# Optimization experiments

Measured on AMD Instinct MI355X. Metric: run time of the kernel, lower is better.

Reference implementation:

```python
import jax, jax.numpy as jnp
import numpy as np

EPS = 1e-5

def _bn_relu(x, gamma, beta):
    # BatchNorm2d in training mode: biased batch stats over (B, H, W)
    mu = jnp.mean(x, axis=(0, 2, 3), keepdims=True)
    var = jnp.mean((x - mu) ** 2, axis=(0, 2, 3), keepdims=True)
    xh = (x - mu) * jax.lax.rsqrt(var + EPS)
    return jax.nn.relu(xh * gamma[None, :, None, None] + beta[None, :, None, None])

def setup_inputs() -> dict:
    key = jax.random.key(0)
    ks = jax.random.split(key, 16)
    B, N, D = 4, 256, 256            # in_channels = 2*D = 512
    feats = jax.random.normal(ks[0], (B, 1 + 2 * N, D), dtype=jnp.float32)
    def lin(k, o, c):
        return jax.random.normal(k, (o, c), dtype=jnp.float32) * (1.0 / np.sqrt(c))
    return {
        "feats": feats,
        "W1": lin(ks[1], 256, 512), "b1": jnp.zeros((256,), jnp.float32),
        "g1": jnp.ones((256,), jnp.float32), "be1": jnp.zeros((256,), jnp.float32),
        "W2": lin(ks[2], 128, 256), "b2": jnp.zeros((128,), jnp.float32),
        "g2": jnp.ones((128,), jnp.float32), "be2": jnp.zeros((128,), jnp.float32),
        "W3": lin(ks[3], 64, 128), "b3": jnp.zeros((64,), jnp.float32),
        "g3": jnp.ones((64,), jnp.float32), "be3": jnp.zeros((64,), jnp.float32),
        "W4": lin(ks[4], 1, 64), "b4": jnp.zeros((1,), jnp.float32),
    }

def reference(feats, W1, b1, g1, be1, W2, b2, g2, be2, W3, b3, g3, be3, W4, b4):
    B, T, Dfull = feats.shape
    f = feats[:, 1:]                                  # [B, 2N, D]
    N = f.shape[1] // 2
    D = f.shape[2]
    f = f.reshape(B, N, 2, D).mean(axis=2)            # [B, N, D]
    fc = jnp.transpose(f, (0, 2, 1))                  # [B, D, N]
    # conv1(cat(x, t)) fused: first D input channels see f_i, last D see f_j
    a = jnp.einsum('oc,bcn->bon', W1[:, :D], fc)      # [B, 256, N]
    bpart = jnp.einsum('oc,bcn->bon', W1[:, D:], fc)  # [B, 256, N]
    h = a[:, :, :, None] + bpart[:, :, None, :] + b1[None, :, None, None]  # [B,256,N,N]
    h = _bn_relu(h, g1, be1)
    h = jnp.einsum('oc,bcij->boij', W2, h) + b2[None, :, None, None]
    h = _bn_relu(h, g2, be2)
    h = jnp.einsum('oc,bcij->boij', W3, h) + b3[None, :, None, None]
    h = _bn_relu(h, g3, be3)
    h = jnp.einsum('oc,bcij->boij', W4, h) + b4[None, :, None, None]
    return h[:, 0]                                    # [B, N, N]
```

## Files before the change

kernel.cpp:

```cpp
#include <hip/hip_runtime.h>
#include <hip/hip_bf16.h>

#define EPS 1e-5f

typedef __attribute__((ext_vector_type(8))) short bf16x8;
typedef __attribute__((ext_vector_type(4))) float f32x4;

static constexpr size_t OFF_FT    = 0;
static constexpr size_t OFF_W1T   = 1048576;
static constexpr size_t OFF_W2B   = 1572864;
static constexpr size_t OFF_W3B   = 1638400;
static constexpr size_t OFF_S1    = 1654784;
static constexpr size_t OFF_T1    = 1655808;
static constexpr size_t OFF_S2    = 1658368;
static constexpr size_t OFF_T2    = 1658880;
static constexpr size_t OFF_S3    = 1659392;
static constexpr size_t OFF_T3    = 1659648;
static constexpr size_t OFF_ST2   = 1660928;
static constexpr size_t OFF_ST3   = 1669120;
static constexpr size_t OFF_ABT   = 1703936;
static constexpr size_t OFF_H2T   = 4194304;
static constexpr size_t OFF_P1    = OFF_H2T;
static constexpr size_t OFF_H3T   = 71303168;

static __device__ inline float bfu2f(unsigned int u16) {
    return __uint_as_float(u16 << 16);
}
static __device__ inline unsigned short f2bfu(float f) {
    unsigned int u = __float_as_uint(f);
    unsigned int r = u + 0x7fffu + ((u >> 16) & 1u);
    return (unsigned short)(r >> 16);
}
static __device__ inline unsigned int pkbf(float lo, float hi) {
    __hip_bfloat162 p = __float22bfloat162_rn(make_float2(lo, hi));
    return *reinterpret_cast<unsigned int*>(&p);
}

__global__ void k0_pairmean_T(const float* __restrict__ feats, float* __restrict__ fT) {
    __shared__ float s[64][65];
    int b = blockIdx.x >> 2;
    int n0 = (blockIdx.x & 3) * 64;
    int tid = threadIdx.x;
    const float* fb = feats + (size_t)b * 513 * 256;
    for (int c0 = 0; c0 < 256; c0 += 64) {
        for (int idx = tid; idx < 64 * 64; idx += 256) {
            int n = idx >> 6, c = idx & 63;
            const float* r = fb + (size_t)(1 + 2 * (n0 + n)) * 256 + c0 + c;
            s[n][c] = 0.5f * (r[0] + r[256]);
        }
        __syncthreads();
        for (int idx = tid; idx < 64 * 64; idx += 256) {
            int c = idx >> 6, n = idx & 63;
            fT[((size_t)b * 256 + c0 + c) * 256 + n0 + n] = s[n][c];
        }
        __syncthreads();
    }
}

__global__ void kt_prep(const float* __restrict__ W1, const float* __restrict__ W2,
                        const float* __restrict__ W3, float* __restrict__ W1T,
                        unsigned short* __restrict__ W2b, unsigned short* __restrict__ W3b) {
    int idx = blockIdx.x * 256 + threadIdx.x;
    if (idx < 131072) {
        int c = idx >> 9, o = idx & 511;
        W1T[idx] = (o < 256) ? W1[(size_t)o * 512 + c] : W1[(size_t)(o - 256) * 512 + 256 + c];
    } else if (idx < 163840) {
        int j = idx - 131072;
        W2b[j] = f2bfu(W2[j]);
    } else if (idx < 172032) {
        int j = idx - 163840;
        W3b[j] = f2bfu(W3[j]);
    }
}

__global__ __launch_bounds__(256) void k1_gemm(const float* __restrict__ W1T,
                                               const float* __restrict__ fT,
                                               float* __restrict__ abT,
                                               float2* __restrict__ part) {
    __shared__ float sW[64][68];
    __shared__ float sF[64][68];
    int tid = threadIdx.x;
    int b = blockIdx.x >> 2, n0 = (blockIdx.x & 3) * 64;
    int o0 = blockIdx.y * 64;
    int jq = tid & 15, og = tid >> 4;
    float acc[4][4] = {};
    for (int c0 = 0; c0 < 256; c0 += 64) {
        for (int idx = tid; idx < 64 * 64; idx += 256) {
            int c = idx >> 6, o = idx & 63;
            sW[c][o] = W1T[(size_t)(c0 + c) * 512 + o0 + o];
        }
        for (int idx = tid; idx < 64 * 64; idx += 256) {
            int c = idx >> 6, n = idx & 63;
            sF[c][n] = fT[((size_t)b * 256 + c0 + c) * 256 + n0 + n];
        }
        __syncthreads();
        #pragma unroll 8
        for (int c = 0; c < 64; ++c) {
            float4 rv = *(const float4*)&sF[c][jq * 4];
            float4 wv = *(const float4*)&sW[c][og * 4];
            float rr[4] = {rv.x, rv.y, rv.z, rv.w};
            float ww[4] = {wv.x, wv.y, wv.z, wv.w};
            #pragma unroll
            for (int m = 0; m < 4; ++m)
                #pragma unroll
                for (int w = 0; w < 4; ++w) acc[m][w] += ww[m] * rr[w];
        }
        __syncthreads();
    }
    for (int w = 0; w < 4; ++w) {
        int n = n0 + jq * 4 + w;
        float4 v = {acc[0][w], acc[1][w], acc[2][w], acc[3][w]};
        *(float4*)&abT[((size_t)(b * 256) + n) * 512 + o0 + og * 4] = v;
    }
    #pragma unroll
    for (int m = 0; m < 4; ++m) {
        float s = 0.f, q = 0.f;
        #pragma unroll
        for (int w = 0; w < 4; ++w) { float v = acc[m][w]; s += v; q += v * v; }
        #pragma unroll
        for (int off = 8; off; off >>= 1) { s += __shfl_down(s, off); q += __shfl_down(q, off); }
        if (jq == 0) part[(size_t)blockIdx.x * 512 + o0 + og * 4 + m] = make_float2(s, q);
    }
}

__global__ void k1b_stats(const float2* __restrict__ part, const float* __restrict__ g1,
                          const float* __restrict__ be1, float* __restrict__ s1,
                          float* __restrict__ t1) {
    __shared__ float Sl[4][512], Ql[4][512];
    int o = threadIdx.x;
    for (int b = 0; b < 4; ++b) {
        float s = 0.f, q = 0.f;
        #pragma unroll
        for (int nt = 0; nt < 4; ++nt) {
            float2 p = part[(size_t)(b * 4 + nt) * 512 + o];
            s += p.x; q += p.y;
        }
        Sl[b][o] = s; Ql[b][o] = q;
    }
    __syncthreads();
    if (o < 256) {
        float msum = 0.f, e2sum = 0.f;
        #pragma unroll
        for (int b = 0; b < 4; ++b) {
            float ma = Sl[b][o] * (1.f / 256.f), mb = Sl[b][o + 256] * (1.f / 256.f);
            msum += ma + mb;
            e2sum += Ql[b][o] * (1.f / 256.f) + Ql[b][o + 256] * (1.f / 256.f) + 2.f * ma * mb;
        }
        float m = msum * 0.25f, e2 = e2sum * 0.25f;
        float var = e2 - m * m;
        float s = g1[o] * rsqrtf(var + EPS);
        s1[o] = s;
        t1[o] = be1[o] - m * s;
    }
}

__global__ __launch_bounds__(256) void k2_mfma(const float* __restrict__ abT,
                                               const unsigned short* __restrict__ W2b,
                                               const float* __restrict__ s1,
                                               const float* __restrict__ t1,
                                               unsigned short* __restrict__ h2T,
                                               float* __restrict__ gS2,
                                               float* __restrict__ gQ2) {
    __shared__ __align__(16) char smem[39936];
    float* aaS = (float*)smem;
    float* ssS = (float*)(smem + 1024);
    unsigned short* sW = (unsigned short*)(smem + 2048);
    unsigned short* sB = (unsigned short*)(smem + 20480);
    float* sS = (float*)(smem + 38912);
    float* sQ = (float*)(smem + 39424);
    unsigned short* sT = (unsigned short*)smem;

    int tid = threadIdx.x;
    int j0 = blockIdx.x * 128, i = blockIdx.y, b = blockIdx.z;

    {
        float av = abT[((size_t)(b * 256 + i)) * 512 + tid];
        float s = s1[tid];
        aaS[tid] = fmaf(av, s, t1[tid]);
        ssS[tid] = s;
    }
    if (tid < 128) { sS[tid] = 0.f; sQ[tid] = 0.f; }
    __syncthreads();

    int lane = tid & 63, wv = tid >> 6;
    int wr = wv >> 1, wc = wv & 1;
    int lo = lane & 15, khi = lane >> 4;

    f32x4 acc[4][4] = {};
    const float* bpB = abT + ((size_t)(b * 256 + j0)) * 512 + 256;

    for (int c0 = 0; c0 < 256; c0 += 64) {
        #pragma unroll
        for (int k = 0; k < 4; ++k) {
            int f = tid + k * 256; int o = f >> 3, cs = f & 7;
            uint4 v = *(const uint4*)(W2b + o * 256 + c0 + cs * 8);
            *(uint4*)(sW + o * 72 + cs * 8) = v;
        }
        #pragma unroll
        for (int k = 0; k < 8; ++k) {
            int f = tid + k * 256; int j = f >> 4, cs = f & 15;
            float4 bp = *(const float4*)(bpB + (size_t)j * 512 + c0 + cs * 4);
            float4 a4 = *(const float4*)&aaS[c0 + cs * 4];
            float4 s4 = *(const float4*)&ssS[c0 + cs * 4];
            float r0 = fmaxf(fmaf(bp.x, s4.x, a4.x), 0.f);
            float r1 = fmaxf(fmaf(bp.y, s4.y, a4.y), 0.f);
            float r2 = fmaxf(fmaf(bp.z, s4.z, a4.z), 0.f);
            float r3 = fmaxf(fmaf(bp.w, s4.w, a4.w), 0.f);
            *(uint2*)(sB + j * 72 + cs * 4) = make_uint2(pkbf(r0, r1), pkbf(r2, r3));
        }
        __syncthreads();
        const unsigned short* aB = sW + (wr * 64 + lo) * 72 + khi * 8;
        const unsigned short* bB = sB + (wc * 64 + lo) * 72 + khi * 8;
        #pragma unroll
        for (int ks = 0; ks < 2; ++ks) {
            bf16x8 af[4], bfr[4];
            #pragma unroll
            for (int fm = 0; fm < 4; ++fm) af[fm] = *(const bf16x8*)(aB + fm * 16 * 72 + ks * 32);
            #pragma unroll
            for (int fn = 0; fn < 4; ++fn) bfr[fn] = *(const bf16x8*)(bB + fn * 16 * 72 + ks * 32);
            #pragma unroll
            for (int fm = 0; fm < 4; ++fm)
                #pragma unroll
                for (int fn = 0; fn < 4; ++fn)
                    acc[fm][fn] = __builtin_amdgcn_mfma_f32_16x16x32_bf16(af[fm], bfr[fn], acc[fm][fn], 0, 0, 0);
        }
        __syncthreads();
    }

    #pragma unroll
    for (int fm = 0; fm < 4; ++fm)
        #pragma unroll
        for (int r = 0; r < 4; ++r) {
            float s = 0.f, q = 0.f;
            #pragma unroll
            for (int fn = 0; fn < 4; ++fn) { float v = acc[fm][fn][r]; s += v; q += v * v; }
            #pragma unroll
            for (int off = 8; off; off >>= 1) { s += __shfl_down(s, off); q += __shfl_down(q, off); }
            if (lo == 0) {
                int o = wr * 64 + fm * 16 + khi * 4 + r;
                atomicAdd(&sS[o], s);
                atomicAdd(&sQ[o], q);
            }
        }
    __syncthreads();

    #pragma unroll
    for (int fm = 0; fm < 4; ++fm)
        #pragma unroll
        for (int fn = 0; fn < 4; ++fn) {
            int oq = wr * 64 + fm * 16 + khi * 4;
            int j  = wc * 64 + fn * 16 + lo;
            unsigned int u0 = pkbf(acc[fm][fn][0], acc[fm][fn][1]);
            unsigned int u1 = pkbf(acc[fm][fn][2], acc[fm][fn][3]);
            *(uint2*)(sT + j * 136 + oq) = make_uint2(u0, u1);
        }
    __syncthreads();
    {
        int jrow = tid >> 1, half = tid & 1;
        size_t gbase = (((size_t)(b * 256 + i)) * 256 + j0 + jrow) * 128 + half * 64;
        #pragma unroll
        for (int e = 0; e < 8; ++e) {
            uint4 v = *(const uint4*)(sT + jrow * 136 + half * 64 + e * 8);
            *(uint4*)(h2T + gbase + e * 8) = v;
        }
    }
    if (tid < 128) {
        int slot = (i & 7) * 128;
        atomicAdd(&gS2[slot + tid], sS[tid]);
        atomicAdd(&gQ2[slot + tid], sQ[tid]);
    }
}

__global__ void kbnparam(const float* __restrict__ gS, const float* __restrict__ gQ,
                         const float* __restrict__ g, const float* __restrict__ be,
                         float* __restrict__ s, float* __restrict__ t, int C, float invc) {
    int o = threadIdx.x;
    if (o < C) {
        float su = 0.f, qu = 0.f;
        #pragma unroll
        for (int k = 0; k < 8; ++k) { su += gS[k * C + o]; qu += gQ[k * C + o]; }
        float mean = su * invc;
        float var = qu * invc - mean * mean;
        float sc = g[o] * rsqrtf(var + EPS);
        s[o] = sc;
        t[o] = be[o] - mean * sc;
    }
}

__global__ __launch_bounds__(256) void k3_mfma(const unsigned short* __restrict__ h2T,
                                               const unsigned short* __restrict__ W3b,
                                               const float* __restrict__ s2,
                                               const float* __restrict__ t2,
                                               unsigned short* __restrict__ h3T,
                                               float* __restrict__ gS3,
                                               float* __restrict__ gQ3) {
    __shared__ __align__(16) char smem[39424];
    float* s2S = (float*)smem;
    float* t2S = (float*)(smem + 512);
    unsigned short* sW3 = (unsigned short*)(smem + 1024);
    unsigned short* sB  = (unsigned short*)(smem + 18432);
    float* sS = (float*)(smem + 38912);
    float* sQ = (float*)(smem + 39168);
    unsigned short* sT  = (unsigned short*)(smem + 1024);

    int tid = threadIdx.x;
    int i = blockIdx.x, b = blockIdx.y;
    if (tid < 128) { s2S[tid] = s2[tid]; t2S[tid] = t2[tid]; }
    if (tid < 64) { sS[tid] = 0.f; sQ[tid] = 0.f; }
    {
        int o = tid >> 2, qd = tid & 3;
        #pragma unroll
        for (int e = 0; e < 4; ++e) {
            uint4 v = *(const uint4*)(W3b + o * 128 + qd * 32 + e * 8);
            *(uint4*)(sW3 + o * 136 + qd * 32 + e * 8) = v;
        }
    }
    __syncthreads();

    int lane = tid & 63, wv = tid >> 6;
    int lo = lane & 15, khi = lane >> 4;

    f32x4 acc[4][4] = {};
    const unsigned short* src = h2T + (((size_t)(b * 256 + i)) * 256 + tid) * 128;

    for (int c0 = 0; c0 < 128; c0 += 32) {
        #pragma unroll
        for (int e = 0; e < 4; ++e) {
            uint4 v = *(const uint4*)(src + c0 + e * 8);
            int c = c0 + e * 8;
            float4 sa = *(const float4*)&s2S[c];
            float4 sb = *(const float4*)&s2S[c + 4];
            float4 ta = *(const float4*)&t2S[c];
            float4 tb = *(const float4*)&t2S[c + 4];
            float r0 = fmaxf(fmaf(bfu2f(v.x & 0xffffu), sa.x, ta.x), 0.f);
            float r1 = fmaxf(fmaf(bfu2f(v.x >> 16),     sa.y, ta.y), 0.f);
            float r2 = fmaxf(fmaf(bfu2f(v.y & 0xffffu), sa.z, ta.z), 0.f);
            float r3 = fmaxf(fmaf(bfu2f(v.y >> 16),     sa.w, ta.w), 0.f);
            float r4 = fmaxf(fmaf(bfu2f(v.z & 0xffffu), sb.x, tb.x), 0.f);
            float r5 = fmaxf(fmaf(bfu2f(v.z >> 16),     sb.y, tb.y), 0.f);
            float r6 = fmaxf(fmaf(bfu2f(v.w & 0xffffu), sb.z, tb.z), 0.f);
            float r7 = fmaxf(fmaf(bfu2f(v.w >> 16),     sb.w, tb.w), 0.f);
            *(uint4*)(sB + tid * 40 + e * 8) =
                make_uint4(pkbf(r0, r1), pkbf(r2, r3), pkbf(r4, r5), pkbf(r6, r7));
        }
        __syncthreads();
        bf16x8 af[4], bfr[4];
        #pragma unroll
        for (int fm = 0; fm < 4; ++fm)
            af[fm] = *(const bf16x8*)(sW3 + (fm * 16 + lo) * 136 + c0 + khi * 8);
        #pragma unroll
        for (int fn = 0; fn < 4; ++fn)
            bfr[fn] = *(const bf16x8*)(sB + (wv * 64 + fn * 16 + lo) * 40 + khi * 8);
        #pragma unroll
        for (int fm = 0; fm < 4; ++fm)
            #pragma unroll
            for (int fn = 0; fn < 4; ++fn)
                acc[fm][fn] = __builtin_amdgcn_mfma_f32_16x16x32_bf16(af[fm], bfr[fn], acc[fm][fn], 0, 0, 0);
        __syncthreads();
    }

    #pragma unroll
    for (int fm = 0; fm < 4; ++fm)
        #pragma unroll
        for (int r = 0; r < 4; ++r) {
            float s = 0.f, q = 0.f;
            #pragma unroll
            for (int fn = 0; fn < 4; ++fn) { float v = acc[fm][fn][r]; s += v; q += v * v; }
            #pragma unroll
            for (int off = 8; off; off >>= 1) { s += __shfl_down(s, off); q += __shfl_down(q, off); }
            if (lo == 0) {
                int o = fm * 16 + khi * 4 + r;
                atomicAdd(&sS[o], s);
                atomicAdd(&sQ[o], q);
            }
        }
    __syncthreads();

    #pragma unroll
    for (int fm = 0; fm < 4; ++fm)
        #pragma unroll
        for (int fn = 0; fn < 4; ++fn) {
            int oq = fm * 16 + khi * 4;
            int j  = wv * 64 + fn * 16 + lo;
            unsigned int u0 = pkbf(acc[fm][fn][0], acc[fm][fn][1]);
            unsigned int u1 = pkbf(acc[fm][fn][2], acc[fm][fn][3]);
            *(uint2*)(sT + j * 72 + oq) = make_uint2(u0, u1);
        }
    __syncthreads();
    {
        size_t gbase = (((size_t)(b * 256 + i)) * 256 + tid) * 64;
        #pragma unroll
        for (int e = 0; e < 8; ++e) {
            uint4 v = *(const uint4*)(sT + tid * 72 + e * 8);
            *(uint4*)(h3T + gbase + e * 8) = v;
        }
    }
    if (tid < 64) {
        int slot = (i & 7) * 64;
        atomicAdd(&gS3[slot + tid], sS[tid]);
        atomicAdd(&gQ3[slot + tid], sQ[tid]);
    }
}

__global__ __launch_bounds__(256) void k4_final(const unsigned short* __restrict__ h3T,
                                                const float* __restrict__ W4,
                                                const float* __restrict__ s3,
                                                const float* __restrict__ t3,
                                                const float* __restrict__ b4,
                                                float* __restrict__ out) {
    __shared__ __align__(16) char smem[37632];
    float* wS = (float*)smem;
    float* sS = (float*)(smem + 256);
    float* tS = (float*)(smem + 512);
    unsigned short* sL = (unsigned short*)(smem + 768);
    int tid = threadIdx.x;
    int i = blockIdx.x, b = blockIdx.y;
    if (tid < 64) { wS[tid] = W4[tid]; sS[tid] = s3[tid]; tS[tid] = t3[tid]; }
    const unsigned short* src = h3T + ((size_t)(b * 256 + i)) * 256 * 64;
    #pragma unroll
    for (int e = 0; e < 8; ++e) {
        int f = tid + 256 * e;
        uint4 v = *(const uint4*)(src + f * 8);
        *(uint4*)(sL + (f >> 3) * 72 + (f & 7) * 8) = v;
    }
    __syncthreads();
    float acc = 0.f;
    #pragma unroll
    for (int e = 0; e < 8; ++e) {
        uint4 v = *(const uint4*)(sL + tid * 72 + e * 8);
        unsigned int w[4] = {v.x, v.y, v.z, v.w};
        #pragma unroll
        for (int k = 0; k < 4; ++k) {
            int c = e * 8 + 2 * k;
            float f0 = bfu2f(w[k] & 0xffffu);
            float f1 = bfu2f(w[k] >> 16);
            acc += wS[c] * fmaxf(fmaf(f0, sS[c], tS[c]), 0.f);
            acc += wS[c + 1] * fmaxf(fmaf(f1, sS[c + 1], tS[c + 1]), 0.f);
        }
    }
    out[((size_t)(b * 256 + i)) * 256 + tid] = acc + b4[0];
}

extern "C" void kernel_launch(void* const* d_in, const int* in_sizes, int n_in,
                              void* d_out, int out_size, void* d_ws, size_t ws_size,
                              hipStream_t stream) {
    const float* feats = (const float*)d_in[0];
    const float* W1  = (const float*)d_in[1];
    const float* g1  = (const float*)d_in[3];
    const float* be1 = (const float*)d_in[4];
    const float* W2  = (const float*)d_in[5];
    const float* g2  = (const float*)d_in[7];
    const float* be2 = (const float*)d_in[8];
    const float* W3  = (const float*)d_in[9];
    const float* g3  = (const float*)d_in[11];
    const float* be3 = (const float*)d_in[12];
    const float* W4  = (const float*)d_in[13];
    const float* b4  = (const float*)d_in[14];

    char* ws = (char*)d_ws;
    float* fT   = (float*)(ws + OFF_FT);
    float* W1T  = (float*)(ws + OFF_W1T);
    unsigned short* W2b = (unsigned short*)(ws + OFF_W2B);
    unsigned short* W3b = (unsigned short*)(ws + OFF_W3B);
    float* abT  = (float*)(ws + OFF_ABT);
    float* s1   = (float*)(ws + OFF_S1);
    float* t1   = (float*)(ws + OFF_T1);
    float* gS2  = (float*)(ws + OFF_ST2);
    float* gQ2  = (float*)(ws + OFF_ST2 + 4096);
    float* gS3  = (float*)(ws + OFF_ST3);
    float* gQ3  = (float*)(ws + OFF_ST3 + 2048);
    float* s2 = (float*)(ws + OFF_S2);
    float* t2 = (float*)(ws + OFF_T2);
    float* s3 = (float*)(ws + OFF_S3);
    float* t3 = (float*)(ws + OFF_T3);
    float2* part = (float2*)(ws + OFF_P1);
    unsigned short* h2T = (unsigned short*)(ws + OFF_H2T);
    unsigned short* h3T = (unsigned short*)(ws + OFF_H3T);
    float* out = (float*)d_out;

    hipMemsetAsync(ws + OFF_ST2, 0, 12288, stream);

    k0_pairmean_T<<<16, 256, 0, stream>>>(feats, fT);
    kt_prep<<<672, 256, 0, stream>>>(W1, W2, W3, W1T, W2b, W3b);
    k1_gemm<<<dim3(16, 8), 256, 0, stream>>>(W1T, fT, abT, part);
    k1b_stats<<<1, 512, 0, stream>>>(part, g1, be1, s1, t1);
    k2_mfma<<<dim3(2, 256, 4), 256, 0, stream>>>(abT, W2b, s1, t1, h2T, gS2, gQ2);
    kbnparam<<<1, 128, 0, stream>>>(gS2, gQ2, g2, be2, s2, t2, 128, 1.f / 262144.f);
    k3_mfma<<<dim3(256, 4), 256, 0, stream>>>(h2T, W3b, s2, t2, h3T, gS3, gQ3);
    kbnparam<<<1, 64, 0, stream>>>(gS3, gQ3, g3, be3, s3, t3, 64, 1.f / 262144.f);
    k4_final<<<dim3(256, 4), 256, 0, stream>>>(h3T, W4, s3, t3, b4, out);
}
```

Before: 241.6 us.

## Fuse prep, stats and BN-param kernels; retile k1 and k2 K-loop

Merges the pair-mean transpose, weight prep and stats-zeroing memset into one kernel. BN1 statistics are folded into the k1 GEMM through a last-block atomic counter, and the BN2/BN3 parameter computation is moved into the prologues of k3 and k4. Together this drops four launches and a memset. k1 now uses 32-wide output tiles, doubling its block count, and k2 uses a 32-wide K step with a smaller shared-memory footprint and per-thread row loads. The trade-offs are a redundant per-block recomputation of BN parameters, a global atomic-counter handoff, and twice as many k2 K iterations and barriers.

```diff
diff --git a/kernel.cpp b/kernel.cpp
--- a/kernel.cpp
+++ b/kernel.cpp
@@ -12,12 +12,7 @@
 static constexpr size_t OFF_W3B   = 1638400;
 static constexpr size_t OFF_S1    = 1654784;
 static constexpr size_t OFF_T1    = 1655808;
-static constexpr size_t OFF_S2    = 1658368;
-static constexpr size_t OFF_T2    = 1658880;
-static constexpr size_t OFF_S3    = 1659392;
-static constexpr size_t OFF_T3    = 1659648;
 static constexpr size_t OFF_ST2   = 1660928;
-static constexpr size_t OFF_ST3   = 1669120;
 static constexpr size_t OFF_ABT   = 1703936;
 static constexpr size_t OFF_H2T   = 4194304;
 static constexpr size_t OFF_P1    = OFF_H2T;
@@ -36,115 +31,153 @@
     return *reinterpret_cast<unsigned int*>(&p);
 }
 
-__global__ void k0_pairmean_T(const float* __restrict__ feats, float* __restrict__ fT) {
-    __shared__ float s[64][65];
-    int b = blockIdx.x >> 2;
-    int n0 = (blockIdx.x & 3) * 64;
-    int tid = threadIdx.x;
-    const float* fb = feats + (size_t)b * 513 * 256;
-    for (int c0 = 0; c0 < 256; c0 += 64) {
-        for (int idx = tid; idx < 64 * 64; idx += 256) {
+static __device__ __forceinline__ uint2 bnpk4(float4 fv, const float* aa, const float* ss, int c) {
+    float4 a4 = *(const float4*)(aa + c);
+    float4 s4 = *(const float4*)(ss + c);
+    float r0 = fmaxf(fmaf(fv.x, s4.x, a4.x), 0.f);
+    float r1 = fmaxf(fmaf(fv.y, s4.y, a4.y), 0.f);
+    float r2 = fmaxf(fmaf(fv.z, s4.z, a4.z), 0.f);
+    float r3 = fmaxf(fmaf(fv.w, s4.w, a4.w), 0.f);
+    return make_uint2(pkbf(r0, r1), pkbf(r2, r3));
+}
+static __device__ __forceinline__ uint2 bn2pk4(uint2 v, const float* ss, const float* tt, int c) {
+    float4 s4 = *(const float4*)(ss + c);
+    float4 t4 = *(const float4*)(tt + c);
+    float r0 = fmaxf(fmaf(bfu2f(v.x & 0xffffu), s4.x, t4.x), 0.f);
+    float r1 = fmaxf(fmaf(bfu2f(v.x >> 16),     s4.y, t4.y), 0.f);
+    float r2 = fmaxf(fmaf(bfu2f(v.y & 0xffffu), s4.z, t4.z), 0.f);
+    float r3 = fmaxf(fmaf(bfu2f(v.y >> 16),     s4.w, t4.w), 0.f);
+    return make_uint2(pkbf(r0, r1), pkbf(r2, r3));
+}
+
+__global__ __launch_bounds__(256) void k0kt(const float* __restrict__ feats,
+                                            const float* __restrict__ W1,
+                                            const float* __restrict__ W2,
+                                            const float* __restrict__ W3,
+                                            float* __restrict__ fT, float* __restrict__ W1T,
+                                            unsigned short* __restrict__ W2b,
+                                            unsigned short* __restrict__ W3b,
+                                            float* __restrict__ statsZero) {
+    int bx = blockIdx.x, tid = threadIdx.x;
+    if (bx < 128) {
+        __shared__ float s[32][65];
+        int b = bx >> 5, nt = (bx >> 2) & 7, ct = bx & 3;
+        int n0 = nt * 32, c0 = ct * 64;
+        const float* fb = feats + (size_t)b * 513 * 256;
+        #pragma unroll
+        for (int k = 0; k < 8; ++k) {
+            int idx = tid + k * 256;
             int n = idx >> 6, c = idx & 63;
             const float* r = fb + (size_t)(1 + 2 * (n0 + n)) * 256 + c0 + c;
             s[n][c] = 0.5f * (r[0] + r[256]);
         }
         __syncthreads();
-        for (int idx = tid; idx < 64 * 64; idx += 256) {
-            int c = idx >> 6, n = idx & 63;
-            fT[((size_t)b * 256 + c0 + c) * 256 + n0 + n] = s[n][c];
-        }
-        __syncthreads();
-    }
-}
-
-__global__ void kt_prep(const float* __restrict__ W1, const float* __restrict__ W2,
-                        const float* __restrict__ W3, float* __restrict__ W1T,
-                        unsigned short* __restrict__ W2b, unsigned short* __restrict__ W3b) {
-    int idx = blockIdx.x * 256 + threadIdx.x;
-    if (idx < 131072) {
-        int c = idx >> 9, o = idx & 511;
-        W1T[idx] = (o < 256) ? W1[(size_t)o * 512 + c] : W1[(size_t)(o - 256) * 512 + 256 + c];
-    } else if (idx < 163840) {
-        int j = idx - 131072;
-        W2b[j] = f2bfu(W2[j]);
-    } else if (idx < 172032) {
-        int j = idx - 163840;
-        W3b[j] = f2bfu(W3[j]);
+        #pragma unroll
+        for (int k = 0; k < 8; ++k) {
+            int idx = tid + k * 256;
+            int c = idx >> 5, n = idx & 31;
+            fT[((size_t)(b * 256) + c0 + c) * 256 + n0 + n] = s[n][c];
+        }
+    } else {
+        if (bx == 128) {
+            #pragma unroll
+            for (int z = 0; z < 13; ++z) {
+                int f = tid + z * 256;
+                if (f < 3073) statsZero[f] = 0.f;
+            }
+        }
+        int idx = (bx - 128) * 256 + tid;
+        if (idx < 131072) {
+            int c = idx >> 9, o = idx & 511;
+            W1T[idx] = (o < 256) ? W1[(size_t)o * 512 + c] : W1[(size_t)(o - 256) * 512 + 256 + c];
+        } else if (idx < 163840) {
+            int j = idx - 131072;
+            W2b[j] = f2bfu(W2[j]);
+        } else if (idx < 172032) {
+            int j = idx - 163840;
+            W3b[j] = f2bfu(W3[j]);
+        }
     }
 }
 
 __global__ __launch_bounds__(256) void k1_gemm(const float* __restrict__ W1T,
                                                const float* __restrict__ fT,
                                                float* __restrict__ abT,
-                                               float2* __restrict__ part) {
-    __shared__ float sW[64][68];
+                                               float2* __restrict__ part,
+                                               const float* __restrict__ g1,
+                                               const float* __restrict__ be1,
+                                               float* __restrict__ s1,
+                                               float* __restrict__ t1,
+                                               unsigned int* __restrict__ counter) {
+    __shared__ float sW[64][36];
     __shared__ float sF[64][68];
     int tid = threadIdx.x;
-    int b = blockIdx.x >> 2, n0 = (blockIdx.x & 3) * 64;
-    int o0 = blockIdx.y * 64;
-    int jq = tid & 15, og = tid >> 4;
-    float acc[4][4] = {};
+    int bx = blockIdx.x;
+    int b = bx >> 2, n0 = (bx & 3) * 64;
+    int o0 = blockIdx.y * 32;
+    int og = tid >> 4, jq = tid & 15;
+    float acc[2][4] = {};
     for (int c0 = 0; c0 < 256; c0 += 64) {
-        for (int idx = tid; idx < 64 * 64; idx += 256) {
-            int c = idx >> 6, o = idx & 63;
+        #pragma unroll
+        for (int k = 0; k < 8; ++k) {
+            int idx = tid + k * 256;
+            int c = idx >> 5, o = idx & 31;
             sW[c][o] = W1T[(size_t)(c0 + c) * 512 + o0 + o];
         }
-        for (int idx = tid; idx < 64 * 64; idx += 256) {
+        #pragma unroll
+        for (int k = 0; k < 16; ++k) {
+            int idx = tid + k * 256;
             int c = idx >> 6, n = idx & 63;
-            sF[c][n] = fT[((size_t)b * 256 + c0 + c) * 256 + n0 + n];
+            sF[c][n] = fT[((size_t)(b * 256) + c0 + c) * 256 + n0 + n];
         }
         __syncthreads();
         #pragma unroll 8
         for (int c = 0; c < 64; ++c) {
             float4 rv = *(const float4*)&sF[c][jq * 4];
-            float4 wv = *(const float4*)&sW[c][og * 4];
+            float2 wv = *(const float2*)&sW[c][og * 2];
             float rr[4] = {rv.x, rv.y, rv.z, rv.w};
-            float ww[4] = {wv.x, wv.y, wv.z, wv.w};
-            #pragma unroll
-            for (int m = 0; m < 4; ++m)
-                #pragma unroll
-                for (int w = 0; w < 4; ++w) acc[m][w] += ww[m] * rr[w];
-        }
-        __syncthreads();
-    }
+            #pragma unroll
+            for (int w = 0; w < 4; ++w) {
+                acc[0][w] = fmaf(wv.x, rr[w], acc[0][w]);
+                acc[1][w] = fmaf(wv.y, rr[w], acc[1][w]);
+            }
+        }
+        __syncthreads();
+    }
+    #pragma unroll
     for (int w = 0; w < 4; ++w) {
         int n = n0 + jq * 4 + w;
-        float4 v = {acc[0][w], acc[1][w], acc[2][w], acc[3][w]};
-        *(float4*)&abT[((size_t)(b * 256) + n) * 512 + o0 + og * 4] = v;
-    }
-    #pragma unroll
-    for (int m = 0; m < 4; ++m) {
+        *(float2*)&abT[((size_t)(b * 256) + n) * 512 + o0 + og * 2] =
+            make_float2(acc[0][w], acc[1][w]);
+    }
+    #pragma unroll
+    for (int m = 0; m < 2; ++m) {
         float s = 0.f, q = 0.f;
         #pragma unroll
         for (int w = 0; w < 4; ++w) { float v = acc[m][w]; s += v; q += v * v; }
         #pragma unroll
         for (int off = 8; off; off >>= 1) { s += __shfl_down(s, off); q += __shfl_down(q, off); }
-        if (jq == 0) part[(size_t)blockIdx.x * 512 + o0 + og * 4 + m] = make_float2(s, q);
-    }
-}
-
-__global__ void k1b_stats(const float2* __restrict__ part, const float* __restrict__ g1,
-                          const float* __restrict__ be1, float* __restrict__ s1,
-                          float* __restrict__ t1) {
-    __shared__ float Sl[4][512], Ql[4][512];
-    int o = threadIdx.x;
-    for (int b = 0; b < 4; ++b) {
-        float s = 0.f, q = 0.f;
-        #pragma unroll
-        for (int nt = 0; nt < 4; ++nt) {
-            float2 p = part[(size_t)(b * 4 + nt) * 512 + o];
-            s += p.x; q += p.y;
-        }
-        Sl[b][o] = s; Ql[b][o] = q;
-    }
-    __syncthreads();
-    if (o < 256) {
+        if (jq == 0) part[(size_t)bx * 512 + o0 + og * 2 + m] = make_float2(s, q);
+    }
+    __threadfence();
+    __shared__ unsigned int lastFlag;
+    if (tid == 0) lastFlag = (atomicAdd(counter, 1u) == 255u) ? 1u : 0u;
+    __syncthreads();
+    if (lastFlag) {
+        int o = tid;
         float msum = 0.f, e2sum = 0.f;
         #pragma unroll
-        for (int b = 0; b < 4; ++b) {
-            float ma = Sl[b][o] * (1.f / 256.f), mb = Sl[b][o + 256] * (1.f / 256.f);
+        for (int bb = 0; bb < 4; ++bb) {
+            float Sa = 0.f, Qa = 0.f, Sb = 0.f, Qb = 0.f;
+            #pragma unroll
+            for (int nt = 0; nt < 4; ++nt) {
+                float2 pa = part[(size_t)(bb * 4 + nt) * 512 + o];
+                float2 pb = part[(size_t)(bb * 4 + nt) * 512 + 256 + o];
+                Sa += pa.x; Qa += pa.y; Sb += pb.x; Qb += pb.y;
+            }
+            float ma = Sa * (1.f / 256.f), mb = Sb * (1.f / 256.f);
             msum += ma + mb;
-            e2sum += Ql[b][o] * (1.f / 256.f) + Ql[b][o + 256] * (1.f / 256.f) + 2.f * ma * mb;
+            e2sum += Qa * (1.f / 256.f) + Qb * (1.f / 256.f) + 2.f * ma * mb;
         }
         float m = msum * 0.25f, e2 = e2sum * 0.25f;
         float var = e2 - m * m;
@@ -161,14 +194,14 @@
                                                unsigned short* __restrict__ h2T,
                                                float* __restrict__ gS2,
                                                float* __restrict__ gQ2) {
-    __shared__ __align__(16) char smem[39936];
+    __shared__ __align__(16) char smem[35840];
     float* aaS = (float*)smem;
     float* ssS = (float*)(smem + 1024);
     unsigned short* sW = (unsigned short*)(smem + 2048);
-    unsigned short* sB = (unsigned short*)(smem + 20480);
-    float* sS = (float*)(smem + 38912);
-    float* sQ = (float*)(smem + 39424);
+    unsigned short* sB = (unsigned short*)(smem + 12288);
     unsigned short* sT = (unsigned short*)smem;
+    float* sS = (float*)(smem + 34816);
+    float* sQ = (float*)(smem + 35328);
 
     int tid = threadIdx.x;
     int j0 = blockIdx.x * 128, i = blockIdx.y, b = blockIdx.z;
@@ -185,45 +218,47 @@
     int lane = tid & 63, wv = tid >> 6;
     int wr = wv >> 1, wc = wv & 1;
     int lo = lane & 15, khi = lane >> 4;
+    int jrow = tid >> 1, half = tid & 1;
+
+    const float* bpRow = abT + ((size_t)(b * 256 + j0 + jrow)) * 512 + 256 + half * 16;
+    const unsigned short* wRow = W2b + jrow * 256 + half * 16;
 
     f32x4 acc[4][4] = {};
-    const float* bpB = abT + ((size_t)(b * 256 + j0)) * 512 + 256;
-
-    for (int c0 = 0; c0 < 256; c0 += 64) {
-        #pragma unroll
-        for (int k = 0; k < 4; ++k) {
-            int f = tid + k * 256; int o = f >> 3, cs = f & 7;
-            uint4 v = *(const uint4*)(W2b + o * 256 + c0 + cs * 8);
-            *(uint4*)(sW + o * 72 + cs * 8) = v;
-        }
-        #pragma unroll
-        for (int k = 0; k < 8; ++k) {
-            int f = tid + k * 256; int j = f >> 4, cs = f & 15;
-            float4 bp = *(const float4*)(bpB + (size_t)j * 512 + c0 + cs * 4);
-            float4 a4 = *(const float4*)&aaS[c0 + cs * 4];
-            float4 s4 = *(const float4*)&ssS[c0 + cs * 4];
-            float r0 = fmaxf(fmaf(bp.x, s4.x, a4.x), 0.f);
-            float r1 = fmaxf(fmaf(bp.y, s4.y, a4.y), 0.f);
-            float r2 = fmaxf(fmaf(bp.z, s4.z, a4.z), 0.f);
-            float r3 = fmaxf(fmaf(bp.w, s4.w, a4.w), 0.f);
-            *(uint2*)(sB + j * 72 + cs * 4) = make_uint2(pkbf(r0, r1), pkbf(r2, r3));
-        }
-        __syncthreads();
-        const unsigned short* aB = sW + (wr * 64 + lo) * 72 + khi * 8;
-        const unsigned short* bB = sB + (wc * 64 + lo) * 72 + khi * 8;
-        #pragma unroll
-        for (int ks = 0; ks < 2; ++ks) {
-            bf16x8 af[4], bfr[4];
-            #pragma unroll
-            for (int fm = 0; fm < 4; ++fm) af[fm] = *(const bf16x8*)(aB + fm * 16 * 72 + ks * 32);
-            #pragma unroll
-            for (int fn = 0; fn < 4; ++fn) bfr[fn] = *(const bf16x8*)(bB + fn * 16 * 72 + ks * 32);
-            #pragma unroll
-            for (int fm = 0; fm < 4; ++fm)
-                #pragma unroll
-                for (int fn = 0; fn < 4; ++fn)
-                    acc[fm][fn] = __builtin_amdgcn_mfma_f32_16x16x32_bf16(af[fm], bfr[fn], acc[fm][fn], 0, 0, 0);
-        }
+
+    for (int c0 = 0; c0 < 256; c0 += 32) {
+        {
+            uint4 v0 = *(const uint4*)(wRow + c0);
+            uint4 v1 = *(const uint4*)(wRow + c0 + 8);
+            uint4* dst = (uint4*)(sW + jrow * 40 + half * 16);
+            dst[0] = v0; dst[1] = v1;
+        }
+        {
+            float4 f0 = *(const float4*)(bpRow + c0);
+            float4 f1 = *(const float4*)(bpRow + c0 + 4);
+            float4 f2 = *(const float4*)(bpRow + c0 + 8);
+            float4 f3 = *(const float4*)(bpRow + c0 + 12);
+            int cb = c0 + half * 16;
+            uint2 p0 = bnpk4(f0, aaS, ssS, cb);
+            uint2 p1 = bnpk4(f1, aaS, ssS, cb + 4);
+            uint2 p2 = bnpk4(f2, aaS, ssS, cb + 8);
+            uint2 p3 = bnpk4(f3, aaS, ssS, cb + 12);
+            uint4* dst = (uint4*)(sB + jrow * 40 + half * 16);
+            dst[0] = make_uint4(p0.x, p0.y, p1.x, p1.y);
+            dst[1] = make_uint4(p2.x, p2.y, p3.x, p3.y);
+        }
+        __syncthreads();
+        const unsigned short* aB = sW + (wr * 64 + lo) * 40 + khi * 8;
+        const unsigned short* bB = sB + (wc * 64 + lo) * 40 + khi * 8;
+        bf16x8 af[4], bfr[4];
+        #pragma unroll
+        for (int fm = 0; fm < 4; ++fm) af[fm] = *(const bf16x8*)(aB + fm * 16 * 40);
+        #pragma unroll
+        for (int fn = 0; fn < 4; ++fn) bfr[fn] = *(const bf16x8*)(bB + fn * 16 * 40);
+        #pragma unroll
+        for (int fm = 0; fm < 4; ++fm)
+            #pragma unroll
+            for (int fn = 0; fn < 4; ++fn)
+                acc[fm][fn] = __builtin_amdgcn_mfma_f32_16x16x32_bf16(af[fm], bfr[fn], acc[fm][fn], 0, 0, 0);
         __syncthreads();
     }
 
@@ -242,7 +277,6 @@
                 atomicAdd(&sQ[o], q);
             }
         }
-    __syncthreads();
 
     #pragma unroll
     for (int fm = 0; fm < 4; ++fm)
@@ -250,13 +284,12 @@
         for (int fn = 0; fn < 4; ++fn) {
             int oq = wr * 64 + fm * 16 + khi * 4;
             int j  = wc * 64 + fn * 16 + lo;
-            unsigned int u0 = pkbf(acc[fm][fn][0], acc[fm][fn][1]);
-            unsigned int u1 = pkbf(acc[fm][fn][2], acc[fm][fn][3]);
-            *(uint2*)(sT + j * 136 + oq) = make_uint2(u0, u1);
+            *(uint2*)(sT + j * 136 + oq) =
+                make_uint2(pkbf(acc[fm][fn][0], acc[fm][fn][1]),
+                           pkbf(acc[fm][fn][2], acc[fm][fn][3]));
         }
     __syncthreads();
     {
-        int jrow = tid >> 1, half = tid & 1;
         size_t gbase = (((size_t)(b * 256 + i)) * 256 + j0 + jrow) * 128 + half * 64;
         #pragma unroll
         for (int e = 0; e < 8; ++e) {
@@ -271,26 +304,12 @@
     }
 }
 
-__global__ void kbnparam(const float* __restrict__ gS, const float* __restrict__ gQ,
-                         const float* __restrict__ g, const float* __restrict__ be,
-                         float* __restrict__ s, float* __restrict__ t, int C, float invc) {
-    int o = threadIdx.x;
-    if (o < C) {
-        float su = 0.f, qu = 0.f;
-        #pragma unroll
-        for (int k = 0; k < 8; ++k) { su += gS[k * C + o]; qu += gQ[k * C + o]; }
-        float mean = su * invc;
-        float var = qu * invc - mean * mean;
-        float sc = g[o] * rsqrtf(var + EPS);
-        s[o] = sc;
-        t[o] = be[o] - mean * sc;
-    }
-}
-
 __global__ __launch_bounds__(256) void k3_mfma(const unsigned short* __restrict__ h2T,
                                                const unsigned short* __restrict__ W3b,
-                                               const float* __restrict__ s2,
-                                               const float* __restrict__ t2,
+                                               const float* __restrict__ gS2,
+                                               const float* __restrict__ gQ2,
+                                               const float* __restrict__ g2,
+                                               const float* __restrict__ be2,
                                                unsigned short* __restrict__ h3T,
                                                float* __restrict__ gS3,
                                                float* __restrict__ gQ3) {
@@ -305,7 +324,16 @@
 
     int tid = threadIdx.x;
     int i = blockIdx.x, b = blockIdx.y;
-    if (tid < 128) { s2S[tid] = s2[tid]; t2S[tid] = t2[tid]; }
+    if (tid < 128) {
+        float su = 0.f, qu = 0.f;
+        #pragma unroll
+        for (int k = 0; k < 8; ++k) { su += gS2[k * 128 + tid]; qu += gQ2[k * 128 + tid]; }
+        float mean = su * (1.f / 262144.f);
+        float var = qu * (1.f / 262144.f) - mean * mean;
+        float sc = g2[tid] * rsqrtf(var + EPS);
+        s2S[tid] = sc;
+        t2S[tid] = be2[tid] - mean * sc;
+    }
     if (tid < 64) { sS[tid] = 0.f; sQ[tid] = 0.f; }
     {
         int o = tid >> 2, qd = tid & 3;
@@ -328,20 +356,9 @@
         for (int e = 0; e < 4; ++e) {
             uint4 v = *(const uint4*)(src + c0 + e * 8);
             int c = c0 + e * 8;
-            float4 sa = *(const float4*)&s2S[c];
-            float4 sb = *(const float4*)&s2S[c + 4];
-            float4 ta = *(const float4*)&t2S[c];
-            float4 tb = *(const float4*)&t2S[c + 4];
-            float r0 = fmaxf(fmaf(bfu2f(v.x & 0xffffu), sa.x, ta.x), 0.f);
-            float r1 = fmaxf(fmaf(bfu2f(v.x >> 16),     sa.y, ta.y), 0.f);
-            float r2 = fmaxf(fmaf(bfu2f(v.y & 0xffffu), sa.z, ta.z), 0.f);
-            float r3 = fmaxf(fmaf(bfu2f(v.y >> 16),     sa.w, ta.w), 0.f);
-            float r4 = fmaxf(fmaf(bfu2f(v.z & 0xffffu), sb.x, tb.x), 0.f);
-            float r5 = fmaxf(fmaf(bfu2f(v.z >> 16),     sb.y, tb.y), 0.f);
-            float r6 = fmaxf(fmaf(bfu2f(v.w & 0xffffu), sb.z, tb.z), 0.f);
-            float r7 = fmaxf(fmaf(bfu2f(v.w >> 16),     sb.w, tb.w), 0.f);
-            *(uint4*)(sB + tid * 40 + e * 8) =
-                make_uint4(pkbf(r0, r1), pkbf(r2, r3), pkbf(r4, r5), pkbf(r6, r7));
+            uint2 pa = bn2pk4(make_uint2(v.x, v.y), s2S, t2S, c);
+            uint2 pb = bn2pk4(make_uint2(v.z, v.w), s2S, t2S, c + 4);
+            *(uint4*)(sB + tid * 40 + e * 8) = make_uint4(pa.x, pa.y, pb.x, pb.y);
         }
         __syncthreads();
         bf16x8 af[4], bfr[4];
@@ -382,9 +399,9 @@
         for (int fn = 0; fn < 4; ++fn) {
             int oq = fm * 16 + khi * 4;
             int j  = wv * 64 + fn * 16 + lo;
-            unsigned int u0 = pkbf(acc[fm][fn][0], acc[fm][fn][1]);
-            unsigned int u1 = pkbf(acc[fm][fn][2], acc[fm][fn][3]);
-            *(uint2*)(sT + j * 72 + oq) = make_uint2(u0, u1);
+            *(uint2*)(sT + j * 72 + oq) =
+                make_uint2(pkbf(acc[fm][fn][0], acc[fm][fn][1]),
+                           pkbf(acc[fm][fn][2], acc[fm][fn][3]));
         }
     __syncthreads();
     {
@@ -404,8 +421,10 @@
 
 __global__ __launch_bounds__(256) void k4_final(const unsigned short* __restrict__ h3T,
                                                 const float* __restrict__ W4,
-                                                const float* __restrict__ s3,
-                                                const float* __restrict__ t3,
+                                                const float* __restrict__ gS3,
+                                                const float* __restrict__ gQ3,
+                                                const float* __restrict__ g3,
+                                                const float* __restrict__ be3,
                                                 const float* __restrict__ b4,
                                                 float* __restrict__ out) {
     __shared__ __align__(16) char smem[37632];
@@ -415,7 +434,17 @@
     unsigned short* sL = (unsigned short*)(smem + 768);
     int tid = threadIdx.x;
     int i = blockIdx.x, b = blockIdx.y;
-    if (tid < 64) { wS[tid] = W4[tid]; sS[tid] = s3[tid]; tS[tid] = t3[tid]; }
+    if (tid < 64) {
+        float su = 0.f, qu = 0.f;
+        #pragma unroll
+        for (int k = 0; k < 8; ++k) { su += gS3[k * 64 + tid]; qu += gQ3[k * 64 + tid]; }
+        float mean = su * (1.f / 262144.f);
+        float var = qu * (1.f / 262144.f) - mean * mean;
+        float sc = g3[tid] * rsqrtf(var + EPS);
+        wS[tid] = W4[tid];
+        sS[tid] = sc;
+        tS[tid] = be3[tid] - mean * sc;
+    }
     const unsigned short* src = h3T + ((size_t)(b * 256 + i)) * 256 * 64;
     #pragma unroll
     for (int e = 0; e < 8; ++e) {
@@ -467,26 +496,17 @@
     float* t1   = (float*)(ws + OFF_T1);
     float* gS2  = (float*)(ws + OFF_ST2);
     float* gQ2  = (float*)(ws + OFF_ST2 + 4096);
-    float* gS3  = (float*)(ws + OFF_ST3);
-    float* gQ3  = (float*)(ws + OFF_ST3 + 2048);
-    float* s2 = (float*)(ws + OFF_S2);
-    float* t2 = (float*)(ws + OFF_T2);
-    float* s3 = (float*)(ws + OFF_S3);
-    float* t3 = (float*)(ws + OFF_T3);
+    float* gS3  = (float*)(ws + OFF_ST2 + 8192);
+    float* gQ3  = (float*)(ws + OFF_ST2 + 10240);
+    unsigned int* counter = (unsigned int*)(ws + OFF_ST2 + 12288);
     float2* part = (float2*)(ws + OFF_P1);
     unsigned short* h2T = (unsigned short*)(ws + OFF_H2T);
     unsigned short* h3T = (unsigned short*)(ws + OFF_H3T);
     float* out = (float*)d_out;
 
-    hipMemsetAsync(ws + OFF_ST2, 0, 12288, stream);
-
-    k0_pairmean_T<<<16, 256, 0, stream>>>(feats, fT);
-    kt_prep<<<672, 256, 0, stream>>>(W1, W2, W3, W1T, W2b, W3b);
-    k1_gemm<<<dim3(16, 8), 256, 0, stream>>>(W1T, fT, abT, part);
-    k1b_stats<<<1, 512, 0, stream>>>(part, g1, be1, s1, t1);
+    k0kt<<<800, 256, 0, stream>>>(feats, W1, W2, W3, fT, W1T, W2b, W3b, (float*)(ws + OFF_ST2));
+    k1_gemm<<<dim3(16, 16), 256, 0, stream>>>(W1T, fT, abT, part, g1, be1, s1, t1, counter);
     k2_mfma<<<dim3(2, 256, 4), 256, 0, stream>>>(abT, W2b, s1, t1, h2T, gS2, gQ2);
-    kbnparam<<<1, 128, 0, stream>>>(gS2, gQ2, g2, be2, s2, t2, 128, 1.f / 262144.f);
-    k3_mfma<<<dim3(256, 4), 256, 0, stream>>>(h2T, W3b, s2, t2, h3T, gS3, gQ3);
-    kbnparam<<<1, 64, 0, stream>>>(gS3, gQ3, g3, be3, s3, t3, 64, 1.f / 262144.f);
-    k4_final<<<dim3(256, 4), 256, 0, stream>>>(h3T, W4, s3, t3, b4, out);
-}
+    k3_mfma<<<dim3(256, 4), 256, 0, stream>>>(h2T, W3b, gS2, gQ2, g2, be2, h3T, gS3, gQ3);
+    k4_final<<<dim3(256, 4), 256, 0, stream>>>(h3T, W4, gS3, gQ3, g3, be3, b4, out);
+}
```

Measured after the change: 245.2 us. No clear change (+1.5%).
